# Optimization experiments

Measured on AMD Instinct MI355X. Metric: run time of the kernel, lower is better.

## Reference

```python
import jax, jax.numpy as jnp
import numpy as np

D_IN, D_K, D_V, N_HEADS = 1024, 64, 64, 16
B, S = 4, 2048


def setup_inputs() -> dict:
    key = jax.random.key(0)
    ks = jax.random.split(key, 9)
    scale = 1.0 / np.sqrt(D_IN)
    return {
        "X": jax.random.normal(ks[0], (B, S, D_IN), dtype=jnp.float32),
        # per-head projection weights, stacked over heads: [H, d_in, d]
        "Wq": jax.random.normal(ks[1], (N_HEADS, D_IN, D_K), dtype=jnp.float32) * scale,
        "bq": jax.random.normal(ks[2], (N_HEADS, D_K), dtype=jnp.float32) * 0.02,
        "Wk": jax.random.normal(ks[3], (N_HEADS, D_IN, D_K), dtype=jnp.float32) * scale,
        "bk": jax.random.normal(ks[4], (N_HEADS, D_K), dtype=jnp.float32) * 0.02,
        "Wv": jax.random.normal(ks[5], (N_HEADS, D_IN, D_V), dtype=jnp.float32) * scale,
        "bv": jax.random.normal(ks[6], (N_HEADS, D_V), dtype=jnp.float32) * 0.02,
        # output projection: [H*d_v, d_in]
        "Wo": jax.random.normal(ks[7], (N_HEADS * D_V, D_IN), dtype=jnp.float32) * (1.0 / np.sqrt(N_HEADS * D_V)),
        "bo": jax.random.normal(ks[8], (D_IN,), dtype=jnp.float32) * 0.02,
    }


def reference(X, Wq, bq, Wk, bk, Wv, bv, Wo, bo):
    # Per-head linear projections, all heads batched: [B,H,S,d]
    Q = jnp.einsum('bsd,hdk->bhsk', X, Wq) + bq[None, :, None, :]
    K = jnp.einsum('bsd,hdk->bhsk', X, Wk) + bk[None, :, None, :]
    V = jnp.einsum('bsd,hdv->bhsv', X, Wv) + bv[None, :, None, :]

    d_k = Q.shape[-1]
    scores = jnp.einsum('bhsk,bhtk->bhst', Q, K) / jnp.sqrt(jnp.float32(d_k))

    S_len = X.shape[1]
    causal = jnp.tril(jnp.ones((S_len, S_len), dtype=bool))  # [S,S]
    scores = jnp.where(causal[None, None, :, :], scores, -jnp.inf)
    P = jax.nn.softmax(scores, axis=-1)

    A = jnp.einsum('bhst,bhtv->bhsv', P, V)        # [B,H,S,d_v]
    # concat heads along feature dim (head-major order matches torch cat over heads)
    A = A.transpose(0, 2, 1, 3).reshape(X.shape[0], S_len, -1)  # [B,S,H*d_v]
    return A @ Wo + bo
```

## Files before the change

kernel.cpp:

```cpp
#include <hip/hip_runtime.h>
#include <cstdint>
#include <cstddef>

typedef __attribute__((ext_vector_type(4))) float f32x4;
typedef __attribute__((ext_vector_type(8))) short s16x8;
typedef __attribute__((ext_vector_type(4))) short s16x4;
typedef __attribute__((ext_vector_type(4))) int i32x4;

#define DEV __device__ __forceinline__

DEV short f2bf(float f) {
    unsigned u = __builtin_bit_cast(unsigned, f);
    unsigned r = (u + 0x7FFFu + ((u >> 16) & 1u)) >> 16;
    return (short)r;
}

DEV float bf2f(short s) {
    return __builtin_bit_cast(float, ((unsigned)(unsigned short)s) << 16);
}

DEV void gload_lds16(const void* g, void* l) {
    __builtin_amdgcn_global_load_lds(
        (const __attribute__((address_space(1))) unsigned int*)g,
        (__attribute__((address_space(3))) unsigned int*)l, 16, 0, 0);
}


__global__ void k_cvt_x(const float* __restrict__ X, short* __restrict__ Xb, int n4) {
    int stride = gridDim.x * blockDim.x;
    for (int i = blockIdx.x * blockDim.x + threadIdx.x; i < n4; i += stride) {
        f32x4 v = *(const f32x4*)&X[i * 4];
        s16x4 s;
#pragma unroll
        for (int j = 0; j < 4; ++j) s[j] = f2bf(v[j]);
        *(s16x4*)&Xb[i * 4] = s;
    }
}

__global__ void k_pack_wqkv_t(const float* __restrict__ Wq, const float* __restrict__ Wk,
                              const float* __restrict__ Wv, short* __restrict__ Wbt) {
    __shared__ float tileT[64][65];
    const int bx = blockIdx.x, tid = threadIdx.x;
    const int t = bx >> 8, h = (bx >> 4) & 15, dc = bx & 15;
    const float* W = (t == 0) ? Wq : (t == 1) ? Wk : Wv;
    const float* src = W + ((size_t)h * 1024 + dc * 64) * 64;
#pragma unroll
    for (int i = 0; i < 4; ++i) {
        int idx4 = i * 256 + tid;
        f32x4 v = *(const f32x4*)&src[idx4 * 4];
        int flat = idx4 * 4;
        int d = flat >> 6, k0 = flat & 63;
#pragma unroll
        for (int q = 0; q < 4; ++q) tileT[k0 + q][d] = v[q];
    }
    __syncthreads();
    const int k = tid >> 2, d4 = (tid & 3) * 16;
    s16x8 o0, o1;
#pragma unroll
    for (int q = 0; q < 8; ++q) {
        o0[q] = f2bf(tileT[k][d4 + q]);
        o1[q] = f2bf(tileT[k][d4 + 8 + q]);
    }
    size_t c = (size_t)t * 1024 + h * 64 + k;
    *(s16x8*)&Wbt[c * 1024 + dc * 64 + d4] = o0;
    *(s16x8*)&Wbt[c * 1024 + dc * 64 + d4 + 8] = o1;
}

__global__ void k_pack_wo_t(const float* __restrict__ Wo, short* __restrict__ Wobt) {
    __shared__ float tileT[64][65];
    const int bx = blockIdx.x, tid = threadIdx.x;
    const int c0 = (bx >> 4) * 64, n0 = (bx & 15) * 64;
    const int r = tid >> 2, cch = tid & 3;
#pragma unroll
    for (int it = 0; it < 4; ++it) {
        int colf = cch * 4 + it * 16;
        f32x4 v = *(const f32x4*)&Wo[(size_t)(c0 + r) * 1024 + n0 + colf];
#pragma unroll
        for (int q = 0; q < 4; ++q) tileT[colf + q][r] = v[q];
    }
    __syncthreads();
    const int n = tid >> 2, c4 = (tid & 3) * 16;
    s16x8 o0, o1;
#pragma unroll
    for (int q = 0; q < 8; ++q) {
        o0[q] = f2bf(tileT[n][c4 + q]);
        o1[q] = f2bf(tileT[n][c4 + 8 + q]);
    }
    *(s16x8*)&Wobt[(size_t)(n0 + n) * 1024 + c0 + c4] = o0;
    *(s16x8*)&Wobt[(size_t)(n0 + n) * 1024 + c0 + c4 + 8] = o1;
}


template <int EPI>
__launch_bounds__(256)
__global__ void gemm_bf16(const short* __restrict__ Ag, const short* __restrict__ Btg,
                          const float* __restrict__ b0, const float* __restrict__ b1,
                          const float* __restrict__ b2,
                          short* __restrict__ O0, short* __restrict__ O1, short* __restrict__ O2,
                          float* __restrict__ Of) {
    __shared__ short As[128 * 64];
    __shared__ short Bs[128 * 64];
    const int tid = threadIdx.x;
    const int wave = tid >> 6, lane = tid & 63;
    const int wm = wave >> 1, wn = wave & 1;
    const int m0 = blockIdx.y * 128, n0 = blockIdx.x * 128;

    f32x4 acc[4][4] = {};

    const int lr = lane >> 3;
    const int cb = (lane & 7) * 16;
    const int cl = cb ^ (lr << 4);

    for (int kt = 0; kt < 16; ++kt) {
        __syncthreads();
#pragma unroll
        for (int i = 0; i < 4; ++i) {
            int r8 = wave * 32 + i * 8;
            const char* ga = (const char*)(Ag + (size_t)(m0 + r8 + lr) * 1024 + kt * 64) + cl;
            gload_lds16(ga, &As[r8 * 64]);
            const char* gb = (const char*)(Btg + (size_t)(n0 + r8 + lr) * 1024 + kt * 64) + cl;
            gload_lds16(gb, &Bs[r8 * 64]);
        }
        asm volatile("s_waitcnt vmcnt(0)" ::: "memory");
        __syncthreads();
#pragma unroll
        for (int ks = 0; ks < 2; ++ks) {
            int kb = ks * 64 + (lane >> 4) * 16;
            s16x8 af[4], bf[4];
#pragma unroll
            for (int mf = 0; mf < 4; ++mf) {
                int m = wm * 64 + mf * 16 + (lane & 15);
                af[mf] = *(const s16x8*)&As[m * 64 + ((kb ^ ((m & 7) << 4)) >> 1)];
            }
#pragma unroll
            for (int nf = 0; nf < 4; ++nf) {
                int n = wn * 64 + nf * 16 + (lane & 15);
                bf[nf] = *(const s16x8*)&Bs[n * 64 + ((kb ^ ((n & 7) << 4)) >> 1)];
            }
#pragma unroll
            for (int mf = 0; mf < 4; ++mf)
#pragma unroll
                for (int nf = 0; nf < 4; ++nf)
                    acc[mf][nf] = __builtin_amdgcn_mfma_f32_16x16x32_bf16(af[mf], bf[nf],
                                                                          acc[mf][nf], 0, 0, 0);
        }
    }

    if (EPI == 0) {
#pragma unroll
        for (int nf = 0; nf < 4; ++nf) {
            int n = n0 + wn * 64 + nf * 16 + (lane & 15);
            int t = n >> 10;
            int h = (n >> 6) & 15;
            int kk = n & 63;
            const float* bias = (t == 0) ? b0 : (t == 1) ? b1 : b2;
            short* dst = (t == 0) ? O0 : (t == 1) ? O1 : O2;
            float scale = (t == 0) ? 0.1803368851f : 1.0f;
            float bb = bias[h * 64 + kk];
#pragma unroll
            for (int mf = 0; mf < 4; ++mf) {
#pragma unroll
                for (int r = 0; r < 4; ++r) {
                    int m = m0 + wm * 64 + mf * 16 + (lane >> 4) * 4 + r;
                    int b_ = m >> 11, sp = m & 2047;
                    float v = (acc[mf][nf][r] + bb) * scale;
                    dst[(((size_t)(b_ * 16 + h)) * 2048 + sp) * 64 + kk] = f2bf(v);
                }
            }
        }
    } else {
#pragma unroll
        for (int nf = 0; nf < 4; ++nf) {
            int n = n0 + wn * 64 + nf * 16 + (lane & 15);
            float bb = b0[n];
#pragma unroll
            for (int mf = 0; mf < 4; ++mf) {
#pragma unroll
                for (int r = 0; r < 4; ++r) {
                    int m = m0 + wm * 64 + mf * 16 + (lane >> 4) * 4 + r;
                    Of[(size_t)m * 1024 + n] = acc[mf][nf][r] + bb;
                }
            }
        }
    }
}


__launch_bounds__(512)
__global__ void gemm_qkv(const short* __restrict__ Ag, const short* __restrict__ Btg,
                         const float* __restrict__ b0, const float* __restrict__ b1,
                         const float* __restrict__ b2,
                         short* __restrict__ O0, short* __restrict__ O1,
                         short* __restrict__ O2) {
    __shared__ short As[256 * 64];
    __shared__ short Bs[128 * 64];
    const int tid = threadIdx.x;
    const int wave = tid >> 6, lane = tid & 63;
    const int wm = wave >> 1, wn = wave & 1;
    const int m0 = blockIdx.y * 256, n0 = blockIdx.x * 128;

    f32x4 acc[4][4] = {};

    const int lr = lane >> 3;
    const int cb = (lane & 7) * 16;
    const int cl = cb ^ (lr << 4);

    for (int kt = 0; kt < 16; ++kt) {
        __syncthreads();
#pragma unroll
        for (int i = 0; i < 4; ++i) {
            int r8 = i * 64 + wave * 8;
            const char* ga = (const char*)(Ag + (size_t)(m0 + r8 + lr) * 1024 + kt * 64) + cl;
            gload_lds16(ga, &As[r8 * 64]);
        }
#pragma unroll
        for (int i = 0; i < 2; ++i) {
            int r8 = i * 64 + wave * 8;
            const char* gb = (const char*)(Btg + (size_t)(n0 + r8 + lr) * 1024 + kt * 64) + cl;
            gload_lds16(gb, &Bs[r8 * 64]);
        }
        asm volatile("s_waitcnt vmcnt(0)" ::: "memory");
        __syncthreads();
#pragma unroll
        for (int ks = 0; ks < 2; ++ks) {
            int kb = ks * 64 + (lane >> 4) * 16;
            s16x8 af[4], bf[4];
#pragma unroll
            for (int mf = 0; mf < 4; ++mf) {
                int m = wm * 64 + mf * 16 + (lane & 15);
                af[mf] = *(const s16x8*)&As[m * 64 + ((kb ^ ((m & 7) << 4)) >> 1)];
            }
#pragma unroll
            for (int nf = 0; nf < 4; ++nf) {
                int n = wn * 64 + nf * 16 + (lane & 15);
                bf[nf] = *(const s16x8*)&Bs[n * 64 + ((kb ^ ((n & 7) << 4)) >> 1)];
            }
#pragma unroll
            for (int mf = 0; mf < 4; ++mf)
#pragma unroll
                for (int nf = 0; nf < 4; ++nf)
                    acc[mf][nf] = __builtin_amdgcn_mfma_f32_16x16x32_bf16(af[mf], bf[nf],
                                                                          acc[mf][nf], 0, 0, 0);
        }
    }

#pragma unroll
    for (int nf = 0; nf < 4; ++nf) {
        int n = n0 + wn * 64 + nf * 16 + (lane & 15);
        int t = n >> 10;
        int h = (n >> 6) & 15;
        int kk = n & 63;
        const float* bias = (t == 0) ? b0 : (t == 1) ? b1 : b2;
        short* dst = (t == 0) ? O0 : (t == 1) ? O1 : O2;
        float scale = (t == 0) ? 0.1803368851f : 1.0f;
        float bb = bias[h * 64 + kk];
#pragma unroll
        for (int mf = 0; mf < 4; ++mf) {
#pragma unroll
            for (int r = 0; r < 4; ++r) {
                int m = m0 + wm * 64 + mf * 16 + (lane >> 4) * 4 + r;
                int b_ = m >> 11, sp = m & 2047;
                float v = (acc[mf][nf][r] + bb) * scale;
                dst[(((size_t)(b_ * 16 + h)) * 2048 + sp) * 64 + kk] = f2bf(v);
            }
        }
    }
}


#define STAGE_K(KT, OFF) do {                                                   \
    _Pragma("unroll")                                                           \
    for (int i_ = 0; i_ < 2; ++i_) {                                            \
        int l_ = wave * 16 + i_ * 8 + lr;          \
        int gr_ = (((l_ >> 4) & 1) << 5) | (((l_ >> 2) & 3) << 3) |             \
                  (((l_ >> 5) & 1) << 2) | (l_ & 3);        \
        const char* g_ = (const char*)(Kb + base + (size_t)((KT) * 64 + gr_) * 64) + cl; \
        gload_lds16(g_, &KsAll[(OFF) + (wave * 16 + i_ * 8) * 64]);             \
    } } while (0)

#define LOAD_V(KT, D0, D1) do {                                                 \
    const short* vs_ = Vb + base + (size_t)((KT) * 64 + 2 * kp) * 64 + vb8 * 8; \
    D0 = *(const s16x8*)vs_;                                                    \
    D1 = *(const s16x8*)(vs_ + 64); } while (0)

#define WRITE_V(OFF, S0, S1) do {                                               \
    _Pragma("unroll")                                                           \
    for (int j_ = 0; j_ < 8; ++j_) {                                            \
        int v_ = vb8 * 8 + j_;                                                  \
        unsigned pk_ = (unsigned)(unsigned short)S0[j_] |                       \
                       ((unsigned)(unsigned short)S1[j_] << 16);                \
        int bo_ = (4 * kp) ^ ((v_ & 7) << 4);                                   \
        *(unsigned*)((char*)&VtAll[(OFF) + v_ * 64] + bo_) = pk_;               \
    } } while (0)

#define RAWEXP(X) asm("v_exp_f32 %0, %1" : "=v"(X) : "v"(X))

#define STRIP2_COMPUTE(KT, OFF) do {                                            \
    f32x4 scL_[4] = {}, scS_[4] = {};                                           \
    __builtin_amdgcn_s_setprio(1);                                              \
    _Pragma("unroll")                                                           \
    for (int ks_ = 0; ks_ < 2; ++ks_) {                                         \
        int kb_ = ks_ * 64 + (lane >> 4) * 16;                                  \
        _Pragma("unroll")                                                       \
        for (int nf_ = 0; nf_ < 4; ++nf_) {                                     \
            int key_ = nf_ * 16 + (lane & 15);                                  \
            s16x8 bf_ = *(const s16x8*)&KsAll[(OFF) + key_ * 64 + ((kb_ ^ ((key_ & 7) << 4)) >> 1)]; \
            scL_[nf_] = __builtin_amdgcn_mfma_f32_16x16x32_bf16(bf_, qL_[ks_], scL_[nf_], 0, 0, 0); \
            scS_[nf_] = __builtin_amdgcn_mfma_f32_16x16x32_bf16(bf_, qS_[ks_], scS_[nf_], 0, 0, 0); \
        }                                                                       \
    }                                                                           \
    __builtin_amdgcn_s_setprio(0);                                              \
    if ((KT) == QTSv_) {                                   \
        int qq_ = wave * 16 + (lane & 15);                                      \
        int g8_ = (lane >> 4) * 8;                                              \
        _Pragma("unroll")                                                       \
        for (int nf_ = 0; nf_ < 4; ++nf_) {                                     \
            _Pragma("unroll")                                                   \
            for (int r_ = 0; r_ < 4; ++r_) {                                    \
                int key_ = ((nf_ & 1) << 5) + g8_ + ((nf_ >> 1) << 2) + r_;     \
                if (key_ > qq_) scS_[nf_][r_] = NEG_INF;                        \
            }                                                                   \
        }                                                                       \
    }                                                                           \
    _Pragma("unroll")                                                           \
    for (int nf_ = 0; nf_ < 4; ++nf_)                                           \
        _Pragma("unroll")                                                       \
        for (int r_ = 0; r_ < 4; ++r_) {                                        \
            RAWEXP(scL_[nf_][r_]);                                              \
            RAWEXP(scS_[nf_][r_]);                                              \
        }                                                                       \
    unsigned pdL_[4][2], pdS_[4][2];                                            \
    _Pragma("unroll")                                                           \
    for (int nf_ = 0; nf_ < 4; ++nf_) {                                         \
        asm("v_cvt_pk_bf16_f32 %0, %1, %2"                                      \
            : "=v"(pdL_[nf_][0]) : "v"(scL_[nf_][0]), "v"(scL_[nf_][1]));       \
        asm("v_cvt_pk_bf16_f32 %0, %1, %2"                                      \
            : "=v"(pdL_[nf_][1]) : "v"(scL_[nf_][2]), "v"(scL_[nf_][3]));       \
        asm("v_cvt_pk_bf16_f32 %0, %1, %2"                                      \
            : "=v"(pdS_[nf_][0]) : "v"(scS_[nf_][0]), "v"(scS_[nf_][1]));       \
        asm("v_cvt_pk_bf16_f32 %0, %1, %2"                                      \
            : "=v"(pdS_[nf_][1]) : "v"(scS_[nf_][2]), "v"(scS_[nf_][3]));       \
    }                                                                           \
    __builtin_amdgcn_s_setprio(1);                                              \
    _Pragma("unroll")                                                           \
    for (int ks_ = 0; ks_ < 2; ++ks_) {                                         \
        i32x4 piL_, piS_;                                                       \
        piL_[0] = (int)pdL_[ks_][0]; piL_[1] = (int)pdL_[ks_][1];               \
        piL_[2] = (int)pdL_[ks_ + 2][0]; piL_[3] = (int)pdL_[ks_ + 2][1];       \
        piS_[0] = (int)pdS_[ks_][0]; piS_[1] = (int)pdS_[ks_][1];               \
        piS_[2] = (int)pdS_[ks_ + 2][0]; piS_[3] = (int)pdS_[ks_ + 2][1];       \
        s16x8 paL_ = __builtin_bit_cast(s16x8, piL_);                           \
        s16x8 paS_ = __builtin_bit_cast(s16x8, piS_);                           \
        lsumL_ = __builtin_amdgcn_mfma_f32_16x16x32_bf16(paL_, onesf, lsumL_, 0, 0, 0); \
        lsumS_ = __builtin_amdgcn_mfma_f32_16x16x32_bf16(paS_, onesf, lsumS_, 0, 0, 0); \
        int kb_ = ks_ * 64 + (lane >> 4) * 16;                                  \
        _Pragma("unroll")                                                       \
        for (int nf_ = 0; nf_ < 4; ++nf_) {                                     \
            int v_ = nf_ * 16 + (lane & 15);                                    \
            s16x8 vf_ = *(const s16x8*)&VtAll[(OFF) + v_ * 64 + ((kb_ ^ ((v_ & 7) << 4)) >> 1)]; \
            oL_[nf_] = __builtin_amdgcn_mfma_f32_16x16x32_bf16(paL_, vf_, oL_[nf_], 0, 0, 0); \
            oS_[nf_] = __builtin_amdgcn_mfma_f32_16x16x32_bf16(paS_, vf_, oS_[nf_], 0, 0, 0); \
        }                                                                       \
    }                                                                           \
    __builtin_amdgcn_s_setprio(0);                                              \
    } while (0)

#define STRIP_COMPUTE(QF, O, LSUM, OFF) do {                                    \
    f32x4 sc_[4] = {};                                                          \
    __builtin_amdgcn_s_setprio(1);                                              \
    _Pragma("unroll")                                                           \
    for (int ks_ = 0; ks_ < 2; ++ks_) {                                         \
        int kb_ = ks_ * 64 + (lane >> 4) * 16;                                  \
        _Pragma("unroll")                                                       \
        for (int nf_ = 0; nf_ < 4; ++nf_) {                                     \
            int key_ = nf_ * 16 + (lane & 15);                                  \
            s16x8 bf_ = *(const s16x8*)&KsAll[(OFF) + key_ * 64 + ((kb_ ^ ((key_ & 7) << 4)) >> 1)]; \
            sc_[nf_] = __builtin_amdgcn_mfma_f32_16x16x32_bf16(bf_, QF[ks_], sc_[nf_], 0, 0, 0); \
        }                                                                       \
    }                                                                           \
    __builtin_amdgcn_s_setprio(0);                                              \
    {                                                                           \
        int qq_ = wave * 16 + (lane & 15);                                      \
        int g8_ = (lane >> 4) * 8;                                              \
        _Pragma("unroll")                                                       \
        for (int nf_ = 0; nf_ < 4; ++nf_) {                                     \
            _Pragma("unroll")                                                   \
            for (int r_ = 0; r_ < 4; ++r_) {                                    \
                int key_ = ((nf_ & 1) << 5) + g8_ + ((nf_ >> 1) << 2) + r_;     \
                if (key_ > qq_) sc_[nf_][r_] = NEG_INF;                         \
            }                                                                   \
        }                                                                       \
    }                                                                           \
    _Pragma("unroll")                                                           \
    for (int nf_ = 0; nf_ < 4; ++nf_)                                           \
        _Pragma("unroll")                                                       \
        for (int r_ = 0; r_ < 4; ++r_) RAWEXP(sc_[nf_][r_]);                    \
    unsigned pd_[4][2];                                                         \
    _Pragma("unroll")                                                           \
    for (int nf_ = 0; nf_ < 4; ++nf_) {                                         \
        asm("v_cvt_pk_bf16_f32 %0, %1, %2"                                      \
            : "=v"(pd_[nf_][0]) : "v"(sc_[nf_][0]), "v"(sc_[nf_][1]));          \
        asm("v_cvt_pk_bf16_f32 %0, %1, %2"                                      \
            : "=v"(pd_[nf_][1]) : "v"(sc_[nf_][2]), "v"(sc_[nf_][3]));          \
    }                                                                           \
    __builtin_amdgcn_s_setprio(1);                                              \
    _Pragma("unroll")                                                           \
    for (int ks_ = 0; ks_ < 2; ++ks_) {                                         \
        i32x4 pi_;                                                              \
        pi_[0] = (int)pd_[ks_][0]; pi_[1] = (int)pd_[ks_][1];                   \
        pi_[2] = (int)pd_[ks_ + 2][0]; pi_[3] = (int)pd_[ks_ + 2][1];           \
        s16x8 pa_ = __builtin_bit_cast(s16x8, pi_);                             \
        LSUM = __builtin_amdgcn_mfma_f32_16x16x32_bf16(pa_, onesf, LSUM, 0, 0, 0); \
        int kb_ = ks_ * 64 + (lane >> 4) * 16;                                  \
        _Pragma("unroll")                                                       \
        for (int nf_ = 0; nf_ < 4; ++nf_) {                                     \
            int v_ = nf_ * 16 + (lane & 15);                                    \
            s16x8 vf_ = *(const s16x8*)&VtAll[(OFF) + v_ * 64 + ((kb_ ^ ((v_ & 7) << 4)) >> 1)]; \
            O[nf_] = __builtin_amdgcn_mfma_f32_16x16x32_bf16(pa_, vf_, O[nf_], 0, 0, 0); \
        }                                                                       \
    }                                                                           \
    __builtin_amdgcn_s_setprio(0);                                              \
    } while (0)

#define ITERB(T, L0, L1, W0, W1) do {                                           \
    const bool st2_ = ((T) + 2 < hi_);                                          \
    if (st2_) { STAGE_K((T) + 2, off2_); LOAD_V((T) + 2, L0, L1); }             \
    STRIP2_COMPUTE((T), off0_);                                                 \
    if ((T) + 1 < hi_) {                                                        \
        WRITE_V(off1_, W0, W1);                                                 \
        if (st2_) asm volatile("s_waitcnt vmcnt(4) lgkmcnt(0)" ::: "memory");   \
        else      asm volatile("s_waitcnt vmcnt(0) lgkmcnt(0)" ::: "memory");   \
        __builtin_amdgcn_s_barrier();                                           \
    }                                                                           \
    int tmp_ = off0_; off0_ = off1_; off1_ = off2_; off2_ = tmp_;               \
} while (0)

#define PEPILOGUE(SOFF, O, LSUM) do {                                           \
    _Pragma("unroll")                                                           \
    for (int r_ = 0; r_ < 4; ++r_) {                                            \
        int row_ = (SOFF) + wave * 16 + (lane >> 4) * 4 + r_;                   \
        if ((lane & 15) == 0) Lp_[row_] = LSUM[r_];                             \
        _Pragma("unroll")                                                       \
        for (int nf_ = 0; nf_ < 4; ++nf_)                                       \
            Op_[row_ * 64 + nf_ * 16 + (lane & 15)] = f2bf(O[nf_][r_]);         \
    } } while (0)

__launch_bounds__(256)
__global__ void attn_fwd(const short* __restrict__ Qb, const short* __restrict__ Kb,
                         const short* __restrict__ Vb, short* __restrict__ Opart,
                         float* __restrict__ Lpart) {
    __shared__ short KsAll[3 * 64 * 64];
    __shared__ short VtAll[3 * 64 * 64];
    const int tid = threadIdx.x, wave = tid >> 6, lane = tid & 63;
    const int hx = blockIdx.x;
    const int y = blockIdx.y;
    const int jj = 15 - (y >> 1);
    const int half = y & 1;
    const int lo_ = half * (jj + 1);
    const int hi_ = lo_ + jj + 1;
    const int QTSv_ = 2 * jj, QTLv_ = 2 * jj + 1;
    const int ND_ = ((hi_ < QTLv_) ? hi_ : QTLv_) - lo_;
    const bool tail_ = (hi_ > QTLv_);
    const size_t base = (size_t)hx * 2048 * 64;
    const float NEG_INF = -__builtin_inff();

    const int qrow = wave * 16 + (lane & 15);
    const int qoff = (lane >> 4) * 8;
    const int lr = lane >> 3, cl = ((lane & 7) * 16) ^ (lr << 4);
    const int kp = tid & 31;
    const int vb8 = tid >> 5;

    const s16x8 onesf = {(short)0x3F80, (short)0x3F80, (short)0x3F80, (short)0x3F80,
                         (short)0x3F80, (short)0x3F80, (short)0x3F80, (short)0x3F80};

    s16x8 qL_[2], qS_[2];
#pragma unroll
    for (int ks = 0; ks < 2; ++ks) {
        qL_[ks] = *(const s16x8*)&Qb[base + (size_t)(QTLv_ * 64 + qrow) * 64 + ks * 32 + qoff];
        qS_[ks] = *(const s16x8*)&Qb[base + (size_t)(QTSv_ * 64 + qrow) * 64 + ks * 32 + qoff];
    }

    f32x4 oL_[4] = {}, oS_[4] = {};
    f32x4 lsumL_ = {}, lsumS_ = {};
    s16x8 vA0_, vA1_, vB0_, vB1_;
    int off0_ = 0, off1_ = 4096, off2_ = 8192;

    STAGE_K(lo_, off0_); LOAD_V(lo_, vA0_, vA1_);
    const bool two_ = (lo_ + 1 < hi_);
    if (two_) { STAGE_K(lo_ + 1, off1_); LOAD_V(lo_ + 1, vB0_, vB1_); }
    WRITE_V(off0_, vA0_, vA1_);
    if (two_) asm volatile("s_waitcnt vmcnt(4) lgkmcnt(0)" ::: "memory");
    else      asm volatile("s_waitcnt vmcnt(0) lgkmcnt(0)" ::: "memory");
    __builtin_amdgcn_s_barrier();

    int t_ = lo_;
    for (; t_ + 1 < lo_ + ND_; t_ += 2) {
        ITERB(t_,     vA0_, vA1_, vB0_, vB1_);
        ITERB(t_ + 1, vB0_, vB1_, vA0_, vA1_);
    }
    if (t_ < lo_ + ND_) { ITERB(t_, vA0_, vA1_, vB0_, vB1_); }

    if (tail_) {
        STRIP_COMPUTE(qL_, oL_, lsumL_, off0_);
    }

    const int slot_ = (hx * 16 + jj) * 2 + half;
    short* Op_ = Opart + (size_t)slot_ * 8192;
    float* Lp_ = Lpart + (size_t)slot_ * 128;
    PEPILOGUE(0, oS_, lsumS_);
    PEPILOGUE(64, oL_, lsumL_);
}

__launch_bounds__(256)
__global__ void attn_combine(const short* __restrict__ Opart, const float* __restrict__ Lpart,
                             short* __restrict__ Ab) {
    const int bx = blockIdx.x, t = threadIdx.x;
    const int hx = bx >> 4, jj = bx & 15;
    const int b_ = hx >> 4, h = hx & 15;
    const short* O0 = Opart + (size_t)((hx * 16 + jj) * 2) * 8192;
    const short* O1 = O0 + 8192;
    const float* L0 = Lpart + (size_t)((hx * 16 + jj) * 2) * 128;
    const float* L1 = L0 + 128;
    const int c4 = (t & 15) * 4;
#pragma unroll
    for (int p = 0; p < 8; ++p) {
        int row = (t >> 4) + p * 16;
        float rl = 1.0f / (L0[row] + L1[row]);
        s16x4 a = *(const s16x4*)&O0[row * 64 + c4];
        s16x4 b = *(const s16x4*)&O1[row * 64 + c4];
        s16x4 o;
#pragma unroll
        for (int q = 0; q < 4; ++q) o[q] = f2bf((bf2f(a[q]) + bf2f(b[q])) * rl);
        int qglob = jj * 128 + row;
        *(s16x4*)&Ab[((size_t)(b_ * 2048 + qglob)) * 1024 + h * 64 + c4] = o;
    }
}


extern "C" void kernel_launch(void* const* d_in, const int* in_sizes, int n_in,
                              void* d_out, int out_size, void* d_ws, size_t ws_size,
                              hipStream_t stream) {
    const float* X  = (const float*)d_in[0];
    const float* Wq = (const float*)d_in[1];
    const float* bq = (const float*)d_in[2];
    const float* Wk = (const float*)d_in[3];
    const float* bk = (const float*)d_in[4];
    const float* Wv = (const float*)d_in[5];
    const float* bv = (const float*)d_in[6];
    const float* Wo = (const float*)d_in[7];
    const float* bo = (const float*)d_in[8];
    float* out = (float*)d_out;
    char* ws = (char*)d_ws;

    short* Wobt  = (short*)(ws);
    short* Qb    = (short*)(ws + 2097152);
    short* Kb    = (short*)(ws + 18874368);
    short* Vb    = (short*)(ws + 35651584);
    short* Ab    = (short*)(ws + 52428800);
    short* Xb    = (short*)(ws + 69206016);
    short* Wbt   = (short*)(ws + 85983232);
    short* Opart = (short*)(ws + 69206016);
    float* Lpart = (float*)(ws + 102760448);

    k_cvt_x<<<2048, 256, 0, stream>>>(X, Xb, 8192 * 1024 / 4);
    k_pack_wqkv_t<<<768, 256, 0, stream>>>(Wq, Wk, Wv, Wbt);
    k_pack_wo_t<<<256, 256, 0, stream>>>(Wo, Wobt);

    gemm_qkv<<<dim3(24, 32), 512, 0, stream>>>(Xb, Wbt, bq, bk, bv, Qb, Kb, Vb);
    attn_fwd<<<dim3(64, 32), 256, 0, stream>>>(Qb, Kb, Vb, Opart, Lpart);
    attn_combine<<<1024, 256, 0, stream>>>(Opart, Lpart, Ab);
    gemm_bf16<1><<<dim3(8, 64), 256, 0, stream>>>(Ab, Wobt, bo, nullptr, nullptr,
                                                  nullptr, nullptr, nullptr, out);
}
```

Measured before the change: 165.4 us.

## Store V transposed from QKV GEMM and stage it via direct global-to-LDS loads

The QKV projection epilogue now writes V in a head-major transposed layout [b,h,d,s]. The attention kernel can then load V^T tiles directly into LDS with global_load_lds, the same way it loads K. This removes the per-iteration register loads and the packed, swizzled LDS writes for V, along with the alternating register buffers, so the loop becomes a simple single-step one. The trade-off is a strided, poorly coalesced scalar store pattern for V in the GEMM epilogue.

```diff
diff --git a/kernel.cpp b/kernel.cpp
--- a/kernel.cpp
+++ b/kernel.cpp
@@ -251,7 +251,6 @@
         int h = (n >> 6) & 15;
         int kk = n & 63;
         const float* bias = (t == 0) ? b0 : (t == 1) ? b1 : b2;
-        short* dst = (t == 0) ? O0 : (t == 1) ? O1 : O2;
         float scale = (t == 0) ? 0.1803368851f : 1.0f;
         float bb = bias[h * 64 + kk];
 #pragma unroll
@@ -261,7 +260,13 @@
                 int m = m0 + wm * 64 + mf * 16 + (lane >> 4) * 4 + r;
                 int b_ = m >> 11, sp = m & 2047;
                 float v = (acc[mf][nf][r] + bb) * scale;
-                dst[(((size_t)(b_ * 16 + h)) * 2048 + sp) * 64 + kk] = f2bf(v);
+                short bfv = f2bf(v);
+                if (t == 2) {
+                    O2[((size_t)((b_ * 16 + h) * 64 + kk)) * 2048 + sp] = bfv;
+                } else {
+                    short* dst = (t == 0) ? O0 : O1;
+                    dst[(((size_t)(b_ * 16 + h)) * 2048 + sp) * 64 + kk] = bfv;
+                }
             }
         }
     }
@@ -278,19 +283,12 @@
         gload_lds16(g_, &KsAll[(OFF) + (wave * 16 + i_ * 8) * 64]);             \
     } } while (0)
 
-#define LOAD_V(KT, D0, D1) do {                                                 \
-    const short* vs_ = Vb + base + (size_t)((KT) * 64 + 2 * kp) * 64 + vb8 * 8; \
-    D0 = *(const s16x8*)vs_;                                                    \
-    D1 = *(const s16x8*)(vs_ + 64); } while (0)
-
-#define WRITE_V(OFF, S0, S1) do {                                               \
-    _Pragma("unroll")                                                           \
-    for (int j_ = 0; j_ < 8; ++j_) {                                            \
-        int v_ = vb8 * 8 + j_;                                                  \
-        unsigned pk_ = (unsigned)(unsigned short)S0[j_] |                       \
-                       ((unsigned)(unsigned short)S1[j_] << 16);                \
-        int bo_ = (4 * kp) ^ ((v_ & 7) << 4);                                   \
-        *(unsigned*)((char*)&VtAll[(OFF) + v_ * 64] + bo_) = pk_;               \
+#define STAGE_V(KT, OFF) do {                                                   \
+    _Pragma("unroll")                                                           \
+    for (int i_ = 0; i_ < 2; ++i_) {                                            \
+        int v_ = wave * 16 + i_ * 8 + lr;          \
+        const char* g_ = (const char*)(VtG + vgh_ + (size_t)v_ * 2048 + (KT) * 64) + cl; \
+        gload_lds16(g_, &VtAll[(OFF) + (wave * 16 + i_ * 8) * 64]);             \
     } } while (0)
 
 #define RAWEXP(X) asm("v_exp_f32 %0, %1" : "=v"(X) : "v"(X))
@@ -422,12 +420,11 @@
     __builtin_amdgcn_s_setprio(0);                                              \
     } while (0)
 
-#define ITERB(T, L0, L1, W0, W1) do {                                           \
+#define ITERB(T) do {                                                           \
     const bool st2_ = ((T) + 2 < hi_);                                          \
-    if (st2_) { STAGE_K((T) + 2, off2_); LOAD_V((T) + 2, L0, L1); }             \
+    if (st2_) { STAGE_K((T) + 2, off2_); STAGE_V((T) + 2, off2_); }             \
     STRIP2_COMPUTE((T), off0_);                                                 \
     if ((T) + 1 < hi_) {                                                        \
-        WRITE_V(off1_, W0, W1);                                                 \
         if (st2_) asm volatile("s_waitcnt vmcnt(4) lgkmcnt(0)" ::: "memory");   \
         else      asm volatile("s_waitcnt vmcnt(0) lgkmcnt(0)" ::: "memory");   \
         __builtin_amdgcn_s_barrier();                                           \
@@ -447,7 +444,7 @@
 
 __launch_bounds__(256)
 __global__ void attn_fwd(const short* __restrict__ Qb, const short* __restrict__ Kb,
-                         const short* __restrict__ Vb, short* __restrict__ Opart,
+                         const short* __restrict__ VtG, short* __restrict__ Opart,
                          float* __restrict__ Lpart) {
     __shared__ short KsAll[3 * 64 * 64];
     __shared__ short VtAll[3 * 64 * 64];
@@ -462,13 +459,12 @@
     const int ND_ = ((hi_ < QTLv_) ? hi_ : QTLv_) - lo_;
     const bool tail_ = (hi_ > QTLv_);
     const size_t base = (size_t)hx * 2048 * 64;
+    const size_t vgh_ = (size_t)hx * 131072;
     const float NEG_INF = -__builtin_inff();
 
     const int qrow = wave * 16 + (lane & 15);
     const int qoff = (lane >> 4) * 8;
     const int lr = lane >> 3, cl = ((lane & 7) * 16) ^ (lr << 4);
-    const int kp = tid & 31;
-    const int vb8 = tid >> 5;
 
     const s16x8 onesf = {(short)0x3F80, (short)0x3F80, (short)0x3F80, (short)0x3F80,
                          (short)0x3F80, (short)0x3F80, (short)0x3F80, (short)0x3F80};
@@ -482,23 +478,21 @@
 
     f32x4 oL_[4] = {}, oS_[4] = {};
     f32x4 lsumL_ = {}, lsumS_ = {};
-    s16x8 vA0_, vA1_, vB0_, vB1_;
     int off0_ = 0, off1_ = 4096, off2_ = 8192;
 
-    STAGE_K(lo_, off0_); LOAD_V(lo_, vA0_, vA1_);
+    STAGE_K(lo_, off0_); STAGE_V(lo_, off0_);
     const bool two_ = (lo_ + 1 < hi_);
-    if (two_) { STAGE_K(lo_ + 1, off1_); LOAD_V(lo_ + 1, vB0_, vB1_); }
-    WRITE_V(off0_, vA0_, vA1_);
-    if (two_) asm volatile("s_waitcnt vmcnt(4) lgkmcnt(0)" ::: "memory");
-    else      asm volatile("s_waitcnt vmcnt(0) lgkmcnt(0)" ::: "memory");
+    if (two_) {
+        STAGE_K(lo_ + 1, off1_); STAGE_V(lo_ + 1, off1_);
+        asm volatile("s_waitcnt vmcnt(4)" ::: "memory");
+    } else {
+        asm volatile("s_waitcnt vmcnt(0)" ::: "memory");
+    }
     __builtin_amdgcn_s_barrier();
 
-    int t_ = lo_;
-    for (; t_ + 1 < lo_ + ND_; t_ += 2) {
-        ITERB(t_,     vA0_, vA1_, vB0_, vB1_);
-        ITERB(t_ + 1, vB0_, vB1_, vA0_, vA1_);
-    }
-    if (t_ < lo_ + ND_) { ITERB(t_, vA0_, vA1_, vB0_, vB1_); }
+    for (int t_ = lo_; t_ < lo_ + ND_; ++t_) {
+        ITERB(t_);
+    }
 
     if (tail_) {
         STRIP_COMPUTE(qL_, oL_, lsumL_, off0_);
@@ -555,7 +549,7 @@
     short* Wobt  = (short*)(ws);
     short* Qb    = (short*)(ws + 2097152);
     short* Kb    = (short*)(ws + 18874368);
-    short* Vb    = (short*)(ws + 35651584);
+    short* VtG   = (short*)(ws + 35651584);
     short* Ab    = (short*)(ws + 52428800);
     short* Xb    = (short*)(ws + 69206016);
     short* Wbt   = (short*)(ws + 85983232);
@@ -566,8 +560,8 @@
     k_pack_wqkv_t<<<768, 256, 0, stream>>>(Wq, Wk, Wv, Wbt);
     k_pack_wo_t<<<256, 256, 0, stream>>>(Wo, Wobt);
 
-    gemm_qkv<<<dim3(24, 32), 512, 0, stream>>>(Xb, Wbt, bq, bk, bv, Qb, Kb, Vb);
-    attn_fwd<<<dim3(64, 32), 256, 0, stream>>>(Qb, Kb, Vb, Opart, Lpart);
+    gemm_qkv<<<dim3(24, 32), 512, 0, stream>>>(Xb, Wbt, bq, bk, bv, Qb, Kb, VtG);
+    attn_fwd<<<dim3(64, 32), 256, 0, stream>>>(Qb, Kb, VtG, Opart, Lpart);
     attn_combine<<<1024, 256, 0, stream>>>(Opart, Lpart, Ab);
     gemm_bf16<1><<<dim3(8, 64), 256, 0, stream>>>(Ab, Wobt, bo, nullptr, nullptr,
                                                   nullptr, nullptr, nullptr, out);
```

After: 190.5 us. 1.15x slower.
